# Optimization experiments

Measured on AMD Instinct MI355X. Metric: run time of the kernel, lower is better.

## Reference

```python
import jax, jax.numpy as jnp
import numpy as np

D = 2048
H = 16
HD = D // H
FF = 4 * D
B, L = 2, 2048
EPS = 1e-6
NEG = -1e9


def setup_inputs() -> dict:
    key = jax.random.key(0)
    ks = jax.random.split(key, 8)
    x = jax.random.normal(ks[0], (B, L, D), dtype=jnp.float32)
    # causal additive mask [1,1,L,L]
    causal = jnp.triu(jnp.full((L, L), NEG, dtype=jnp.float32), k=1)
    mask = causal[None, None, :, :]
    s = 0.02
    params = {
        'norm1_w': jnp.ones((D,), jnp.float32),
        'qkv_w': jax.random.normal(ks[1], (3 * D, D), jnp.float32) * s,
        'out_w': jax.random.normal(ks[2], (D, D), jnp.float32) * s,
        'norm2_w': jnp.ones((D,), jnp.float32),
        'gate_w': jax.random.normal(ks[3], (FF, D), jnp.float32) * s,
        'up_w': jax.random.normal(ks[4], (FF, D), jnp.float32) * s,
        'down_w': jax.random.normal(ks[5], (D, FF), jnp.float32) * s,
    }
    return {'x': x, 'mask': mask, **params}


def _rmsnorm(x, w):
    return x * jax.lax.rsqrt(jnp.mean(x * x, axis=-1, keepdims=True) + EPS) * w


def reference(x, mask, norm1_w, qkv_w, out_w, norm2_w, gate_w, up_w, down_w):
    b, l, d = x.shape
    # --- attention ---
    h = _rmsnorm(x, norm1_w)
    qkv = h @ qkv_w.T                          # [B,L,3D]
    qkv = qkv.reshape(b, l, 3, H, HD)
    q, k, v = (jnp.moveaxis(qkv, 2, 0)[i].transpose(0, 2, 1, 3) for i in range(3))  # each [B,H,L,HD]
    scores = jnp.einsum('bhqd,bhkd->bhqk', q, k) / jnp.sqrt(jnp.float32(HD))
    scores = scores + mask
    attn = jax.nn.softmax(scores, axis=-1)
    o = jnp.einsum('bhqk,bhkd->bhqd', attn, v)  # [B,H,L,HD]
    o = o.transpose(0, 2, 1, 3).reshape(b, l, d)
    x = x + o @ out_w.T
    # --- SwiGLU FFN ---
    h2 = _rmsnorm(x, norm2_w)
    ff = (jax.nn.silu(h2 @ gate_w.T) * (h2 @ up_w.T)) @ down_w.T
    return x + ff
```

## Files before the change

### kernel.cpp

```cpp
#include <hip/hip_runtime.h>


typedef __attribute__((ext_vector_type(8))) short bf16x8;
typedef __attribute__((ext_vector_type(4))) float f32x4;

__device__ __forceinline__ float b2f(unsigned short u) {
    return __uint_as_float(((unsigned int)u) << 16);
}
__device__ __forceinline__ unsigned short f2b(float f) {
    unsigned int i = __float_as_uint(f);
    i += 0x7fffu + ((i >> 16) & 1u);
    return (unsigned short)(i >> 16);
}
__device__ __forceinline__ unsigned int cvt_pk_bf16(float lo, float hi) {
    unsigned int r;
    asm("v_cvt_pk_bf16_f32 %0, %1, %2" : "=v"(r) : "v"(lo), "v"(hi));
    return r;
}

__device__ __forceinline__ void gload_lds16(const unsigned short* g, unsigned short* l) {
    __builtin_amdgcn_global_load_lds(
        (const __attribute__((address_space(1))) unsigned int*)g,
        (__attribute__((address_space(3))) unsigned int*)l,
        16, 0, 0);
}

template<int DT> struct IO;
template<> struct IO<1> {
    static __device__ __forceinline__ void load8(const void* p, size_t i, float* o) {
        uint4 v = *(const uint4*)((const unsigned short*)p + i);
        const unsigned short* u = (const unsigned short*)&v;
#pragma unroll
        for (int e = 0; e < 8; e++) o[e] = b2f(u[e]);
    }
    static __device__ __forceinline__ float load1(const void* p, size_t i) {
        return b2f(((const unsigned short*)p)[i]);
    }
    static __device__ __forceinline__ void store1(void* p, size_t i, float v) {
        ((unsigned short*)p)[i] = f2b(v);
    }
};
template<> struct IO<0> {
    static __device__ __forceinline__ void load8(const void* p, size_t i, float* o) {
        float4 a = *(const float4*)((const float*)p + i);
        float4 b = *(const float4*)((const float*)p + i + 4);
        o[0]=a.x; o[1]=a.y; o[2]=a.z; o[3]=a.w;
        o[4]=b.x; o[5]=b.y; o[6]=b.z; o[7]=b.w;
    }
    static __device__ __forceinline__ float load1(const void* p, size_t i) {
        return ((const float*)p)[i];
    }
    static __device__ __forceinline__ void store1(void* p, size_t i, float v) {
        ((float*)p)[i] = v;
    }
};

__global__ __launch_bounds__(256) void detect_kernel(
    const unsigned int* __restrict__ x, int* __restrict__ flag)
{
    const int t = threadIdx.x;
    int cnt = 0;
    for (int i = t; i < 2048; i += 256) {
        unsigned int e = (x[i] >> 7) & 0xFFu;
        cnt += (e >= 100u && e <= 140u) ? 1 : 0;
    }
#pragma unroll
    for (int off = 32; off; off >>= 1) cnt += __shfl_xor(cnt, off);
    __shared__ int red[4];
    if ((t & 63) == 0) red[t >> 6] = cnt;
    __syncthreads();
    if (t == 0) {
        int tot = red[0] + red[1] + red[2] + red[3];
        flag[0] = (2 * tot > 2048) ? 1 : 0;
    }
}

template<int PID, int DTX, int DTW>
__global__ __launch_bounds__(256) void rmsnorm_kernel(
    const int* __restrict__ flag,
    const void* __restrict__ X,
    const void* __restrict__ Wn,
    unsigned short* __restrict__ Out)
{
    if (flag[0] != PID) return;
    const int row = blockIdx.x, t = threadIdx.x;
    float xf[8];
    IO<DTX>::load8(X, (size_t)row * 2048 + t * 8, xf);
    float ss = 0.f;
#pragma unroll
    for (int e = 0; e < 8; e++) ss += xf[e] * xf[e];
#pragma unroll
    for (int off = 32; off; off >>= 1) ss += __shfl_xor(ss, off);
    __shared__ float red[4];
    if ((t & 63) == 0) red[t >> 6] = ss;
    __syncthreads();
    float rr = rsqrtf((red[0] + red[1] + red[2] + red[3]) * (1.0f / 2048.0f) + 1e-6f);
    float wf[8];
    IO<DTW>::load8(Wn, (size_t)t * 8, wf);
    float y[8];
#pragma unroll
    for (int e = 0; e < 8; e++) y[e] = xf[e] * rr * wf[e];
    uint4 ov;
    ov.x = cvt_pk_bf16(y[0], y[1]);
    ov.y = cvt_pk_bf16(y[2], y[3]);
    ov.z = cvt_pk_bf16(y[4], y[5]);
    ov.w = cvt_pk_bf16(y[6], y[7]);
    *(uint4*)(Out + (size_t)row * 2048 + t * 8) = ov;
}

#define BM 128
#define BN 128
#define BKK 64

template<int PID, int DTW, int DTR, int DTC, int EPI>
__global__ __launch_bounds__(256) void gemm_bt(
    const int* __restrict__ flag,
    const unsigned short* __restrict__ A,
    const void* __restrict__ W, size_t woff, int ldw,
    const void* __restrict__ Res,
    void* __restrict__ C,
    int N, int K)
{
    if (flag[0] != PID) return;
    __shared__ unsigned short sA[BM * BKK];
    __shared__ unsigned short sB[BN * BKK];
    const int t = threadIdx.x;
    const int bm = blockIdx.x * BM, bn = blockIdx.y * BN;
    const int w = t >> 6, lane = t & 63, quad = lane >> 4, l16 = lane & 15;
    const int wm = (w & 1) * 64, wn = (w >> 1) * 64;

    const int srow = lane >> 3;
    const int sg   = (lane & 7) ^ srow;

    f32x4 acc[4][4];
#pragma unroll
    for (int mi = 0; mi < 4; mi++)
#pragma unroll
        for (int ni = 0; ni < 4; ni++) {
            f32x4 z = {0.f, 0.f, 0.f, 0.f};
            acc[mi][ni] = z;
        }

    for (int k0 = 0; k0 < K; k0 += BKK) {
#pragma unroll
        for (int i = 0; i < 4; i++) {
            const int r0 = w * 32 + i * 8;
            gload_lds16(A + (size_t)(bm + r0 + srow) * K + k0 + sg * 8,
                        &sA[r0 * BKK]);
        }
        if constexpr (DTW == 1) {
#pragma unroll
            for (int i = 0; i < 4; i++) {
                const int r0 = w * 32 + i * 8;
                gload_lds16((const unsigned short*)W + woff +
                                (size_t)(bn + r0 + srow) * ldw + k0 + sg * 8,
                            &sB[r0 * BKK]);
            }
        } else {
#pragma unroll
            for (int i = 0; i < 4; i++) {
                const int r0 = w * 32 + i * 8;
                const int r = r0 + srow;
                const float* gp = (const float*)W + woff +
                                  (size_t)(bn + r) * ldw + k0 + (lane & 7) * 8;
                float4 f0 = *(const float4*)gp;
                float4 f1 = *(const float4*)(gp + 4);
                uint4 wb;
                wb.x = cvt_pk_bf16(f0.x, f0.y);
                wb.y = cvt_pk_bf16(f0.z, f0.w);
                wb.z = cvt_pk_bf16(f1.x, f1.y);
                wb.w = cvt_pk_bf16(f1.z, f1.w);
                *(uint4*)&sB[r * BKK + (((lane & 7) ^ (r & 7)) * 8)] = wb;
            }
        }
        __syncthreads();

#pragma unroll
        for (int ks = 0; ks < 2; ks++) {
            bf16x8 af[4], bfr[4];
#pragma unroll
            for (int mi = 0; mi < 4; mi++) {
                const int r = wm + mi * 16 + l16;
                af[mi] = *(const bf16x8*)
                    &sA[r * BKK + (((ks * 4 + quad) ^ (r & 7)) * 8)];
            }
#pragma unroll
            for (int ni = 0; ni < 4; ni++) {
                const int r = wn + ni * 16 + l16;
                bfr[ni] = *(const bf16x8*)
                    &sB[r * BKK + (((ks * 4 + quad) ^ (r & 7)) * 8)];
            }
#pragma unroll
            for (int mi = 0; mi < 4; mi++)
#pragma unroll
                for (int ni = 0; ni < 4; ni++)
                    acc[mi][ni] = __builtin_amdgcn_mfma_f32_16x16x32_bf16(
                        af[mi], bfr[ni], acc[mi][ni], 0, 0, 0);
        }
        __syncthreads();
    }

#pragma unroll
    for (int mi = 0; mi < 4; mi++)
#pragma unroll
        for (int ni = 0; ni < 4; ni++)
#pragma unroll
            for (int r = 0; r < 4; r++) {
                const int row = bm + wm + mi * 16 + quad * 4 + r;
                const int col = bn + wn + ni * 16 + l16;
                const size_t idx = (size_t)row * N + col;
                float v = acc[mi][ni][r];
                if constexpr (EPI == 1) v += IO<DTR>::load1(Res, idx);
                if constexpr (EPI == 2) v = v / (1.f + __expf(-v));
                if constexpr (EPI == 3) v *= IO<DTR>::load1(Res, idx);
                IO<DTC>::store1(C, idx, v);
            }
}

__device__ __forceinline__ int vt_idx(int d, int kv) {
    return d * 72 + (kv ^ (d & 56));
}

template<int PID>
__global__ __launch_bounds__(256) void attn_kernel(
    const int* __restrict__ flag,
    const unsigned short* __restrict__ QKV,
    unsigned short* __restrict__ O)
{
    if (flag[0] != PID) return;
    __shared__ unsigned short sK[64 * 128];
    __shared__ unsigned short sVt[9280];
    __shared__ unsigned short sP[4][16 * 72];

    const int t = threadIdx.x;
    const int bh = blockIdx.x >> 4;
    const int jj = blockIdx.x & 15;
    const int b = bh >> 4, hh = bh & 15;
    const int w = t >> 6, lane = t & 63, quad = lane >> 4, l16 = lane & 15;

    const unsigned short* Qb = QKV + (size_t)(b * 2048) * 6144 + hh * 128;
    const unsigned short* Kb = Qb + 2048;
    const unsigned short* Vb = Qb + 4096;

    const int str = t >> 4;
    const int stc = (t & 15) * 8;

#pragma unroll
    for (int half = 0; half < 2; half++) {
        const int qt = half ? (31 - jj) : jj;
        const int qbase = qt * 64;

        bf16x8 qf[4];
        {
            const unsigned short* qp = Qb + (size_t)(qbase + w * 16 + l16) * 6144;
#pragma unroll
            for (int ks = 0; ks < 4; ks++)
                qf[ks] = *(const bf16x8*)(qp + ks * 32 + quad * 8);
        }

        float m[4], l[4];
#pragma unroll
        for (int r = 0; r < 4; r++) { m[r] = -1e30f; l[r] = 0.f; }
        f32x4 accO[8];
#pragma unroll
        for (int d0 = 0; d0 < 8; d0++) {
            f32x4 z = {0.f, 0.f, 0.f, 0.f};
            accO[d0] = z;
        }

        for (int tk = 0; tk <= qt; tk++) {
            const int kv0 = tk * 64;
            __syncthreads();
#pragma unroll
            for (int pass = 0; pass < 4; pass++) {
                const int rr = str + pass * 16;
                uint4 kv4 = *(const uint4*)(Kb + (size_t)(kv0 + rr) * 6144 + stc);
                *(uint4*)&sK[(rr * 128 + stc) ^ ((rr & 7) << 3)] = kv4;
                uint4 vv4 = *(const uint4*)(Vb + (size_t)(kv0 + rr) * 6144 + stc);
                const unsigned short* vu = (const unsigned short*)&vv4;
#pragma unroll
                for (int e = 0; e < 8; e++)
                    sVt[vt_idx(stc + e, rr)] = vu[e];
            }
            __syncthreads();

            const bool diag = (tk == qt);
            f32x4 s[4];
#pragma unroll
            for (int nf = 0; nf < 4; nf++) {
                f32x4 z = {0.f, 0.f, 0.f, 0.f};
                s[nf] = z;
                if (!(diag && nf > w)) {
#pragma unroll
                    for (int ks = 0; ks < 4; ks++) {
                        const int row = nf * 16 + l16;
                        bf16x8 kf = *(const bf16x8*)
                            &sK[(row * 128 + ks * 32 + quad * 8) ^ ((row & 7) << 3)];
                        s[nf] = __builtin_amdgcn_mfma_f32_16x16x32_bf16(qf[ks], kf, s[nf], 0, 0, 0);
                    }
                }
#pragma unroll
                for (int r = 0; r < 4; r++) s[nf][r] *= 0.08838834764831845f;
            }
            if (diag) {
#pragma unroll
                for (int nf = 0; nf < 4; nf++)
#pragma unroll
                    for (int r = 0; r < 4; r++)
                        if (nf * 16 + l16 > w * 16 + quad * 4 + r) s[nf][r] = -1e30f;
            }

            float alpha[4], rs[4];
#pragma unroll
            for (int r = 0; r < 4; r++) {
                float v = fmaxf(fmaxf(s[0][r], s[1][r]), fmaxf(s[2][r], s[3][r]));
                v = fmaxf(v, __shfl_xor(v, 1));
                v = fmaxf(v, __shfl_xor(v, 2));
                v = fmaxf(v, __shfl_xor(v, 4));
                v = fmaxf(v, __shfl_xor(v, 8));
                float mn = fmaxf(m[r], v);
                alpha[r] = __expf(m[r] - mn);
                m[r] = mn;
                rs[r] = 0.f;
            }
#pragma unroll
            for (int nf = 0; nf < 4; nf++)
#pragma unroll
                for (int r = 0; r < 4; r++) {
                    float p = __expf(s[nf][r] - m[r]);
                    rs[r] += p;
                    sP[w][(quad * 4 + r) * 72 + nf * 16 + l16] = f2b(p);
                }
#pragma unroll
            for (int r = 0; r < 4; r++) {
                float sum = rs[r];
                sum += __shfl_xor(sum, 1);
                sum += __shfl_xor(sum, 2);
                sum += __shfl_xor(sum, 4);
                sum += __shfl_xor(sum, 8);
                l[r] = l[r] * alpha[r] + sum;
            }
#pragma unroll
            for (int d0 = 0; d0 < 8; d0++)
#pragma unroll
                for (int r = 0; r < 4; r++) accO[d0][r] *= alpha[r];

#pragma unroll
            for (int ks = 0; ks < 2; ks++) {
                bf16x8 pa = *(const bf16x8*)&sP[w][l16 * 72 + ks * 32 + quad * 8];
#pragma unroll
                for (int d0 = 0; d0 < 8; d0++) {
                    bf16x8 vb = *(const bf16x8*)
                        &sVt[vt_idx(d0 * 16 + l16, ks * 32 + quad * 8)];
                    accO[d0] = __builtin_amdgcn_mfma_f32_16x16x32_bf16(pa, vb, accO[d0], 0, 0, 0);
                }
            }
        }

        float linv[4];
#pragma unroll
        for (int r = 0; r < 4; r++) linv[r] = 1.0f / l[r];
        unsigned short* Op = O + (size_t)(b * 2048 + qbase + w * 16) * 2048 + hh * 128;
#pragma unroll
        for (int d0 = 0; d0 < 8; d0++)
#pragma unroll
            for (int r = 0; r < 4; r++)
                Op[(size_t)(quad * 4 + r) * 2048 + d0 * 16 + l16] =
                    f2b(accO[d0][r] * linv[r]);
    }
}

template<int DT>
static void run_pipeline(const void* x, const void* n1w, const void* qkvw,
                         const void* outw, const void* n2w, const void* gatew,
                         const void* upw, const void* downw,
                         void* outp, char* ws, const int* flag, hipStream_t stream)
{
    const size_t MB = 1024 * 1024;
    unsigned short* qkv = (unsigned short*)(ws);
    unsigned short* x2  = (unsigned short*)(ws);
    unsigned short* h2  = (unsigned short*)(ws + 16 * MB);
    unsigned short* a   = (unsigned short*)(ws + 32 * MB);
    unsigned short* h   = (unsigned short*)(ws + 48 * MB);
    unsigned short* o   = (unsigned short*)(ws + 48 * MB);

    rmsnorm_kernel<DT, DT, DT><<<4096, 256, 0, stream>>>(flag, x, n1w, h);
    gemm_bt<DT, DT, 1, 1, 0><<<dim3(32, 48), 256, 0, stream>>>(
        flag, h, qkvw, 0, 2048, nullptr, qkv, 6144, 2048);
    attn_kernel<DT><<<512, 256, 0, stream>>>(flag, qkv, o);
    gemm_bt<DT, DT, DT, 1, 1><<<dim3(32, 16), 256, 0, stream>>>(
        flag, o, outw, 0, 2048, x, x2, 2048, 2048);
    rmsnorm_kernel<DT, 1, DT><<<4096, 256, 0, stream>>>(flag, x2, n2w, h2);
    gemm_bt<DT, DT, 1, 1, 2><<<dim3(32, 32), 256, 0, stream>>>(
        flag, h2, gatew, 0, 2048, nullptr, a, 4096, 2048);
    gemm_bt<DT, DT, 1, 1, 3><<<dim3(32, 32), 256, 0, stream>>>(
        flag, h2, upw, 0, 2048, a, a, 4096, 2048);
    gemm_bt<DT, DT, 1, 1, 1><<<dim3(32, 16), 256, 0, stream>>>(
        flag, a, downw, 0, 8192, x2, x2, 2048, 4096);
    gemm_bt<DT, DT, 1, 1, 2><<<dim3(32, 32), 256, 0, stream>>>(
        flag, h2, gatew, (size_t)4096 * 2048, 2048, nullptr, a, 4096, 2048);
    gemm_bt<DT, DT, 1, 1, 3><<<dim3(32, 32), 256, 0, stream>>>(
        flag, h2, upw, (size_t)4096 * 2048, 2048, a, a, 4096, 2048);
    gemm_bt<DT, DT, 1, DT, 1><<<dim3(32, 16), 256, 0, stream>>>(
        flag, a, downw, 4096, 8192, x2, outp, 2048, 4096);
}

extern "C" void kernel_launch(void* const* d_in, const int* in_sizes, int n_in,
                              void* d_out, int out_size, void* d_ws, size_t ws_size,
                              hipStream_t stream)
{
    const void* x      = d_in[0];
    const void* n1w    = d_in[2];
    const void* qkv_w  = d_in[3];
    const void* out_w  = d_in[4];
    const void* n2w    = d_in[5];
    const void* gate_w = d_in[6];
    const void* up_w   = d_in[7];
    const void* down_w = d_in[8];

    char* ws = (char*)d_ws;
    const size_t MB = 1024 * 1024;
    size_t flag_off = 64 * MB;
    if (ws_size < flag_off + 4) flag_off = (ws_size - 4) & ~(size_t)3;
    int* flag = (int*)(ws + flag_off);

    detect_kernel<<<1, 256, 0, stream>>>((const unsigned int*)x, flag);
    run_pipeline<0>(x, n1w, qkv_w, out_w, n2w, gate_w, up_w, down_w,
                    d_out, ws, flag, stream);
    run_pipeline<1>(x, n1w, qkv_w, out_w, n2w, gate_w, up_w, down_w,
                    d_out, ws, flag, stream);
}
```

Before: 1.290 ms.

## Add 256x256 double-buffered GEMM with XCD swizzle for bf16 path

Adds a new GEMM kernel for the bf16-input path. It uses 256x256 tiles over 512 threads, double-buffers LDS and interleaves the next tile's global->LDS loads with MFMA phases. Block indices are remapped so that consecutive tiles land on the same XCD. All bf16 GEMMs in the pipeline now use it, while the fp32 path keeps the old kernel. The larger tile raises reuse per byte loaded, but launches fewer workgroups (128–384) on the many CUs and adds barrier and register pressure.

```diff
diff --git a/kernel.cpp b/kernel.cpp
--- a/kernel.cpp
+++ b/kernel.cpp
@@ -106,6 +106,199 @@
     ov.z = cvt_pk_bf16(y[4], y[5]);
     ov.w = cvt_pk_bf16(y[6], y[7]);
     *(uint4*)(Out + (size_t)row * 2048 + t * 8) = ov;
+}
+
+#define TBM 256
+#define TBN 256
+#define TBK 64
+
+template<int PID, int EPI>
+__global__ __launch_bounds__(512, 2) void gemm8(
+    const int* __restrict__ flag,
+    const unsigned short* __restrict__ A,
+    const unsigned short* __restrict__ W, size_t woff, int ldw,
+    const unsigned short* __restrict__ Res,
+    unsigned short* __restrict__ C,
+    int N, int K, int gx)
+{
+    if (flag[0] != PID) return;
+    __shared__ unsigned short sA[2][TBM * TBK];
+    __shared__ unsigned short sB[2][TBN * TBK];
+
+    const int t = threadIdx.x;
+    const int nwg = gridDim.x;
+    const int q8 = nwg >> 3, r8 = nwg & 7;
+    const int xcd = blockIdx.x & 7, o = blockIdx.x >> 3;
+    const int swz = (xcd < r8 ? xcd * (q8 + 1) : r8 * (q8 + 1) + (xcd - r8) * q8) + o;
+    const int bm = (swz % gx) * TBM;
+    const int bn = (swz / gx) * TBN;
+
+    const int w = t >> 6, lane = t & 63, quad = lane >> 4, l16 = lane & 15;
+    const int wr = w >> 2, wc = w & 3;
+    const int sg = (lane & 7) ^ (lane >> 3);
+
+    const unsigned short* Ab = A + (size_t)(bm + w * 8 + (lane >> 3)) * K + sg * 8;
+    const unsigned short* Wb = W + woff + (size_t)(bn + w * 8 + (lane >> 3)) * ldw + sg * 8;
+    const int dstb = (w * 8) * TBK;
+
+    f32x4 acc[8][4];
+#pragma unroll
+    for (int mi = 0; mi < 8; mi++)
+#pragma unroll
+        for (int ni = 0; ni < 4; ni++) {
+            f32x4 z = {0.f, 0.f, 0.f, 0.f};
+            acc[mi][ni] = z;
+        }
+
+#define STAGE_A8(b, k0)                                                        \
+    {                                                                          \
+        _Pragma("unroll")                                                      \
+        for (int i = 0; i < 4; i++)                                            \
+            gload_lds16(Ab + (size_t)(i * 64) * K + (k0),                      \
+                        &sA[b][i * 64 * TBK + dstb]);                          \
+    }
+#define STAGE_B8(b, k0)                                                        \
+    {                                                                          \
+        _Pragma("unroll")                                                      \
+        for (int i = 0; i < 4; i++)                                            \
+            gload_lds16(Wb + (size_t)(i * 64) * ldw + (k0),                    \
+                        &sB[b][i * 64 * TBK + dstb]);                          \
+    }
+
+    STAGE_A8(0, 0)
+    STAGE_B8(0, 0)
+    asm volatile("s_waitcnt vmcnt(0)" ::: "memory");
+    asm volatile("s_barrier" ::: "memory");
+
+    const int NT = K / TBK;
+    bf16x8 bfr[4][2];
+
+    for (int T = 0; T < NT; T++) {
+        const int buf = T & 1;
+        const int k0n = (T + 1) * TBK;
+        const bool more = (T + 1 < NT);
+
+        if (more) STAGE_A8(buf ^ 1, k0n)
+#pragma unroll
+        for (int ni = 0; ni < 4; ni++) {
+            const int row = wc * 64 + ni * 16 + l16;
+#pragma unroll
+            for (int ks = 0; ks < 2; ks++)
+                bfr[ni][ks] = *(const bf16x8*)
+                    &sB[buf][row * TBK + (((ks * 4 + quad) ^ (row & 7)) * 8)];
+        }
+        {
+            bf16x8 af[2][2];
+#pragma unroll
+            for (int m2 = 0; m2 < 2; m2++) {
+                const int row = wr * 128 + (0 + m2) * 16 + l16;
+#pragma unroll
+                for (int ks = 0; ks < 2; ks++)
+                    af[m2][ks] = *(const bf16x8*)
+                        &sA[buf][row * TBK + (((ks * 4 + quad) ^ (row & 7)) * 8)];
+            }
+            __builtin_amdgcn_s_setprio(1);
+#pragma unroll
+            for (int m2 = 0; m2 < 2; m2++)
+#pragma unroll
+                for (int ks = 0; ks < 2; ks++)
+#pragma unroll
+                    for (int ni = 0; ni < 4; ni++)
+                        acc[0 + m2][ni] = __builtin_amdgcn_mfma_f32_16x16x32_bf16(
+                            af[m2][ks], bfr[ni][ks], acc[0 + m2][ni], 0, 0, 0);
+            __builtin_amdgcn_s_setprio(0);
+        }
+        asm volatile("s_barrier" ::: "memory");
+
+        if (more) STAGE_B8(buf ^ 1, k0n)
+        {
+            bf16x8 af[2][2];
+#pragma unroll
+            for (int m2 = 0; m2 < 2; m2++) {
+                const int row = wr * 128 + (2 + m2) * 16 + l16;
+#pragma unroll
+                for (int ks = 0; ks < 2; ks++)
+                    af[m2][ks] = *(const bf16x8*)
+                        &sA[buf][row * TBK + (((ks * 4 + quad) ^ (row & 7)) * 8)];
+            }
+            __builtin_amdgcn_s_setprio(1);
+#pragma unroll
+            for (int m2 = 0; m2 < 2; m2++)
+#pragma unroll
+                for (int ks = 0; ks < 2; ks++)
+#pragma unroll
+                    for (int ni = 0; ni < 4; ni++)
+                        acc[2 + m2][ni] = __builtin_amdgcn_mfma_f32_16x16x32_bf16(
+                            af[m2][ks], bfr[ni][ks], acc[2 + m2][ni], 0, 0, 0);
+            __builtin_amdgcn_s_setprio(0);
+        }
+        asm volatile("s_barrier" ::: "memory");
+
+        {
+            bf16x8 af[2][2];
+#pragma unroll
+            for (int m2 = 0; m2 < 2; m2++) {
+                const int row = wr * 128 + (4 + m2) * 16 + l16;
+#pragma unroll
+                for (int ks = 0; ks < 2; ks++)
+                    af[m2][ks] = *(const bf16x8*)
+                        &sA[buf][row * TBK + (((ks * 4 + quad) ^ (row & 7)) * 8)];
+            }
+            __builtin_amdgcn_s_setprio(1);
+#pragma unroll
+            for (int m2 = 0; m2 < 2; m2++)
+#pragma unroll
+                for (int ks = 0; ks < 2; ks++)
+#pragma unroll
+                    for (int ni = 0; ni < 4; ni++)
+                        acc[4 + m2][ni] = __builtin_amdgcn_mfma_f32_16x16x32_bf16(
+                            af[m2][ks], bfr[ni][ks], acc[4 + m2][ni], 0, 0, 0);
+            __builtin_amdgcn_s_setprio(0);
+        }
+        asm volatile("s_barrier" ::: "memory");
+
+        {
+            bf16x8 af[2][2];
+#pragma unroll
+            for (int m2 = 0; m2 < 2; m2++) {
+                const int row = wr * 128 + (6 + m2) * 16 + l16;
+#pragma unroll
+                for (int ks = 0; ks < 2; ks++)
+                    af[m2][ks] = *(const bf16x8*)
+                        &sA[buf][row * TBK + (((ks * 4 + quad) ^ (row & 7)) * 8)];
+            }
+            __builtin_amdgcn_s_setprio(1);
+#pragma unroll
+            for (int m2 = 0; m2 < 2; m2++)
+#pragma unroll
+                for (int ks = 0; ks < 2; ks++)
+#pragma unroll
+                    for (int ni = 0; ni < 4; ni++)
+                        acc[6 + m2][ni] = __builtin_amdgcn_mfma_f32_16x16x32_bf16(
+                            af[m2][ks], bfr[ni][ks], acc[6 + m2][ni], 0, 0, 0);
+            __builtin_amdgcn_s_setprio(0);
+        }
+        asm volatile("s_waitcnt vmcnt(0)" ::: "memory");
+        asm volatile("s_barrier" ::: "memory");
+    }
+#undef STAGE_A8
+#undef STAGE_B8
+
+#pragma unroll
+    for (int mi = 0; mi < 8; mi++)
+#pragma unroll
+        for (int ni = 0; ni < 4; ni++)
+#pragma unroll
+            for (int r = 0; r < 4; r++) {
+                const int row = bm + wr * 128 + mi * 16 + quad * 4 + r;
+                const int col = bn + wc * 64 + ni * 16 + l16;
+                const size_t idx = (size_t)row * N + col;
+                float v = acc[mi][ni][r];
+                if constexpr (EPI == 1) v += b2f(Res[idx]);
+                if constexpr (EPI == 2) v = v / (1.f + __expf(-v));
+                if constexpr (EPI == 3) v *= b2f(Res[idx]);
+                C[idx] = f2b(v);
+            }
 }
 
 #define BM 128
@@ -141,11 +334,12 @@
             acc[mi][ni] = z;
         }
 
+    const unsigned short* Ap = A;
     for (int k0 = 0; k0 < K; k0 += BKK) {
 #pragma unroll
         for (int i = 0; i < 4; i++) {
             const int r0 = w * 32 + i * 8;
-            gload_lds16(A + (size_t)(bm + r0 + srow) * K + k0 + sg * 8,
+            gload_lds16(Ap + (size_t)(bm + r0 + srow) * K + k0 + sg * 8,
                         &sA[r0 * BKK]);
         }
         if constexpr (DTW == 1) {
@@ -385,24 +579,51 @@
     unsigned short* o   = (unsigned short*)(ws + 48 * MB);
 
     rmsnorm_kernel<DT, DT, DT><<<4096, 256, 0, stream>>>(flag, x, n1w, h);
-    gemm_bt<DT, DT, 1, 1, 0><<<dim3(32, 48), 256, 0, stream>>>(
-        flag, h, qkvw, 0, 2048, nullptr, qkv, 6144, 2048);
-    attn_kernel<DT><<<512, 256, 0, stream>>>(flag, qkv, o);
-    gemm_bt<DT, DT, DT, 1, 1><<<dim3(32, 16), 256, 0, stream>>>(
-        flag, o, outw, 0, 2048, x, x2, 2048, 2048);
-    rmsnorm_kernel<DT, 1, DT><<<4096, 256, 0, stream>>>(flag, x2, n2w, h2);
-    gemm_bt<DT, DT, 1, 1, 2><<<dim3(32, 32), 256, 0, stream>>>(
-        flag, h2, gatew, 0, 2048, nullptr, a, 4096, 2048);
-    gemm_bt<DT, DT, 1, 1, 3><<<dim3(32, 32), 256, 0, stream>>>(
-        flag, h2, upw, 0, 2048, a, a, 4096, 2048);
-    gemm_bt<DT, DT, 1, 1, 1><<<dim3(32, 16), 256, 0, stream>>>(
-        flag, a, downw, 0, 8192, x2, x2, 2048, 4096);
-    gemm_bt<DT, DT, 1, 1, 2><<<dim3(32, 32), 256, 0, stream>>>(
-        flag, h2, gatew, (size_t)4096 * 2048, 2048, nullptr, a, 4096, 2048);
-    gemm_bt<DT, DT, 1, 1, 3><<<dim3(32, 32), 256, 0, stream>>>(
-        flag, h2, upw, (size_t)4096 * 2048, 2048, a, a, 4096, 2048);
-    gemm_bt<DT, DT, 1, DT, 1><<<dim3(32, 16), 256, 0, stream>>>(
-        flag, a, downw, 4096, 8192, x2, outp, 2048, 4096);
+
+    if constexpr (DT == 1) {
+        const unsigned short* Wq = (const unsigned short*)qkvw;
+        const unsigned short* Wo = (const unsigned short*)outw;
+        const unsigned short* Wg = (const unsigned short*)gatew;
+        const unsigned short* Wu = (const unsigned short*)upw;
+        const unsigned short* Wd = (const unsigned short*)downw;
+        gemm8<1, 0><<<384, 512, 0, stream>>>(
+            flag, h, Wq, 0, 2048, nullptr, qkv, 6144, 2048, 16);
+        attn_kernel<1><<<512, 256, 0, stream>>>(flag, qkv, o);
+        gemm8<1, 1><<<128, 512, 0, stream>>>(
+            flag, o, Wo, 0, 2048, (const unsigned short*)x, x2, 2048, 2048, 16);
+        rmsnorm_kernel<1, 1, 1><<<4096, 256, 0, stream>>>(flag, x2, n2w, h2);
+        gemm8<1, 2><<<256, 512, 0, stream>>>(
+            flag, h2, Wg, 0, 2048, nullptr, a, 4096, 2048, 16);
+        gemm8<1, 3><<<256, 512, 0, stream>>>(
+            flag, h2, Wu, 0, 2048, a, a, 4096, 2048, 16);
+        gemm8<1, 1><<<128, 512, 0, stream>>>(
+            flag, a, Wd, 0, 8192, x2, x2, 2048, 4096, 16);
+        gemm8<1, 2><<<256, 512, 0, stream>>>(
+            flag, h2, Wg, (size_t)4096 * 2048, 2048, nullptr, a, 4096, 2048, 16);
+        gemm8<1, 3><<<256, 512, 0, stream>>>(
+            flag, h2, Wu, (size_t)4096 * 2048, 2048, a, a, 4096, 2048, 16);
+        gemm8<1, 1><<<128, 512, 0, stream>>>(
+            flag, a, Wd, 4096, 8192, x2, (unsigned short*)outp, 2048, 4096, 16);
+    } else {
+        gemm_bt<0, 0, 1, 1, 0><<<dim3(32, 48), 256, 0, stream>>>(
+            flag, h, qkvw, 0, 2048, nullptr, qkv, 6144, 2048);
+        attn_kernel<0><<<512, 256, 0, stream>>>(flag, qkv, o);
+        gemm_bt<0, 0, 0, 1, 1><<<dim3(32, 16), 256, 0, stream>>>(
+            flag, o, outw, 0, 2048, x, x2, 2048, 2048);
+        rmsnorm_kernel<0, 1, 0><<<4096, 256, 0, stream>>>(flag, x2, n2w, h2);
+        gemm_bt<0, 0, 1, 1, 2><<<dim3(32, 32), 256, 0, stream>>>(
+            flag, h2, gatew, 0, 2048, nullptr, a, 4096, 2048);
+        gemm_bt<0, 0, 1, 1, 3><<<dim3(32, 32), 256, 0, stream>>>(
+            flag, h2, upw, 0, 2048, a, a, 4096, 2048);
+        gemm_bt<0, 0, 1, 1, 1><<<dim3(32, 16), 256, 0, stream>>>(
+            flag, a, downw, 0, 8192, x2, x2, 2048, 4096);
+        gemm_bt<0, 0, 1, 1, 2><<<dim3(32, 32), 256, 0, stream>>>(
+            flag, h2, gatew, (size_t)4096 * 2048, 2048, nullptr, a, 4096, 2048);
+        gemm_bt<0, 0, 1, 1, 3><<<dim3(32, 32), 256, 0, stream>>>(
+            flag, h2, upw, (size_t)4096 * 2048, 2048, a, a, 4096, 2048);
+        gemm_bt<0, 0, 1, 0, 1><<<dim3(32, 16), 256, 0, stream>>>(
+            flag, a, downw, 4096, 8192, x2, outp, 2048, 4096);
+    }
 }
 
 extern "C" void kernel_launch(void* const* d_in, const int* in_sizes, int n_in,
```

New measurement: 1.287 ms. No clear change (-0.2%).

## Replace GEMM with triple-buffered 512-thread kernel and pre-convert fp32 weights

Applied to the files above, without the earlier changes.

Replaces the single-buffered 128x128 GEMM with a 512-thread kernel using 256-wide N tiles, BK=32 and a three-stage global-to-LDS pipeline with explicit vmcnt waits. It also adds an XCD-aware block swizzle and raises MFMA priority around the math. For fp32 weights, a separate conversion kernel writes bf16 copies into scratch (reusing the output and h2 buffers) before each GEMM, instead of converting inside the tile loop. This adds extra weight read and write traffic, and reusing those buffers depends on the kernels running in order.

```diff
diff --git a/kernel.cpp b/kernel.cpp
--- a/kernel.cpp
+++ b/kernel.cpp
@@ -73,6 +73,28 @@
         int tot = red[0] + red[1] + red[2] + red[3];
         flag[0] = (2 * tot > 2048) ? 1 : 0;
     }
+}
+
+template<int PID>
+__global__ __launch_bounds__(256) void convw_kernel(
+    const int* __restrict__ flag,
+    const float* __restrict__ S, int lds_,
+    unsigned short* __restrict__ D, int ldd,
+    int total)
+{
+    if (flag[0] != PID) return;
+    const int i = (blockIdx.x * 256 + threadIdx.x) * 8;
+    if (i >= total) return;
+    const int row = i / ldd, col = i - row * ldd;
+    const float* sp = S + (size_t)row * lds_ + col;
+    float4 f0 = *(const float4*)sp;
+    float4 f1 = *(const float4*)(sp + 4);
+    uint4 ov;
+    ov.x = cvt_pk_bf16(f0.x, f0.y);
+    ov.y = cvt_pk_bf16(f0.z, f0.w);
+    ov.z = cvt_pk_bf16(f1.x, f1.y);
+    ov.w = cvt_pk_bf16(f1.z, f1.w);
+    *(uint4*)(D + i) = ov;
 }
 
 template<int PID, int DTX, int DTW>
@@ -108,106 +130,110 @@
     *(uint4*)(Out + (size_t)row * 2048 + t * 8) = ov;
 }
 
-#define BM 128
-#define BN 128
-#define BKK 64
-
-template<int PID, int DTW, int DTR, int DTC, int EPI>
-__global__ __launch_bounds__(256) void gemm_bt(
+template<int PID, int TBMX, int DTR, int DTC, int EPI>
+__global__ __launch_bounds__(512, 2) void gemm3(
     const int* __restrict__ flag,
     const unsigned short* __restrict__ A,
-    const void* __restrict__ W, size_t woff, int ldw,
+    const unsigned short* __restrict__ W, size_t woff, int ldw,
     const void* __restrict__ Res,
     void* __restrict__ C,
-    int N, int K)
+    int N, int K, int gx)
 {
     if (flag[0] != PID) return;
-    __shared__ unsigned short sA[BM * BKK];
-    __shared__ unsigned short sB[BN * BKK];
+    constexpr int MF  = TBMX / 32;
+    constexpr int ACH = TBMX / 128;
+    constexpr int LPT = ACH + 2;
+    __shared__ unsigned short sA[3][TBMX * 32];
+    __shared__ unsigned short sB[3][256 * 32];
+
     const int t = threadIdx.x;
-    const int bm = blockIdx.x * BM, bn = blockIdx.y * BN;
+    const int nwg = gridDim.x;
+    const int q8 = nwg >> 3, r8 = nwg & 7;
+    const int xcd = blockIdx.x & 7, oo = blockIdx.x >> 3;
+    const int swz = (xcd < r8 ? xcd * (q8 + 1) : r8 * (q8 + 1) + (xcd - r8) * q8) + oo;
+    const int bm = (swz % gx) * TBMX;
+    const int bn = (swz / gx) * 256;
+
     const int w = t >> 6, lane = t & 63, quad = lane >> 4, l16 = lane & 15;
-    const int wm = (w & 1) * 64, wn = (w >> 1) * 64;
-
-    const int srow = lane >> 3;
-    const int sg   = (lane & 7) ^ srow;
-
-    f32x4 acc[4][4];
-#pragma unroll
-    for (int mi = 0; mi < 4; mi++)
+    const int wr = w >> 2, wc = w & 3;
+    const int swr = (l16 ^ (l16 >> 2)) & 3;
+
+    const int srow = w * 16 + (lane >> 2);
+    const int sgr  = (((t & 3) ^ ((lane >> 2) & 3) ^ quad) << 3);
+    const unsigned short* Abase = A + (size_t)(bm + srow) * K + sgr;
+    const unsigned short* Wbase = W + woff + (size_t)(bn + srow) * ldw + sgr;
+    const int ldst = w * 512;
+
+    f32x4 acc[MF][4];
+#pragma unroll
+    for (int mi = 0; mi < MF; mi++)
 #pragma unroll
         for (int ni = 0; ni < 4; ni++) {
             f32x4 z = {0.f, 0.f, 0.f, 0.f};
             acc[mi][ni] = z;
         }
 
-    for (int k0 = 0; k0 < K; k0 += BKK) {
-#pragma unroll
-        for (int i = 0; i < 4; i++) {
-            const int r0 = w * 32 + i * 8;
-            gload_lds16(A + (size_t)(bm + r0 + srow) * K + k0 + sg * 8,
-                        &sA[r0 * BKK]);
-        }
-        if constexpr (DTW == 1) {
-#pragma unroll
-            for (int i = 0; i < 4; i++) {
-                const int r0 = w * 32 + i * 8;
-                gload_lds16((const unsigned short*)W + woff +
-                                (size_t)(bn + r0 + srow) * ldw + k0 + sg * 8,
-                            &sB[r0 * BKK]);
-            }
+#define STG(bb, T)                                                             \
+    do {                                                                       \
+        const size_t ko = (size_t)(T) * 32;                                    \
+        _Pragma("unroll")                                                      \
+        for (int c = 0; c < ACH; c++)                                          \
+            gload_lds16(Abase + (size_t)(c * 128) * K + ko,                    \
+                        &sA[bb][c * 4096 + ldst]);                             \
+        _Pragma("unroll")                                                      \
+        for (int c = 0; c < 2; c++)                                            \
+            gload_lds16(Wbase + (size_t)(c * 128) * ldw + ko,                  \
+                        &sB[bb][c * 4096 + ldst]);                             \
+    } while (0)
+
+    STG(0, 0);
+    STG(1, 1);
+
+    const int NT = K / 32;
+    for (int T = 0; T < NT; T++) {
+        if (T + 1 < NT) {
+            if constexpr (LPT == 4)
+                asm volatile("s_waitcnt vmcnt(4)" ::: "memory");
+            else
+                asm volatile("s_waitcnt vmcnt(3)" ::: "memory");
         } else {
-#pragma unroll
-            for (int i = 0; i < 4; i++) {
-                const int r0 = w * 32 + i * 8;
-                const int r = r0 + srow;
-                const float* gp = (const float*)W + woff +
-                                  (size_t)(bn + r) * ldw + k0 + (lane & 7) * 8;
-                float4 f0 = *(const float4*)gp;
-                float4 f1 = *(const float4*)(gp + 4);
-                uint4 wb;
-                wb.x = cvt_pk_bf16(f0.x, f0.y);
-                wb.y = cvt_pk_bf16(f0.z, f0.w);
-                wb.z = cvt_pk_bf16(f1.x, f1.y);
-                wb.w = cvt_pk_bf16(f1.z, f1.w);
-                *(uint4*)&sB[r * BKK + (((lane & 7) ^ (r & 7)) * 8)] = wb;
-            }
-        }
-        __syncthreads();
-
-#pragma unroll
-        for (int ks = 0; ks < 2; ks++) {
-            bf16x8 af[4], bfr[4];
-#pragma unroll
-            for (int mi = 0; mi < 4; mi++) {
-                const int r = wm + mi * 16 + l16;
-                af[mi] = *(const bf16x8*)
-                    &sA[r * BKK + (((ks * 4 + quad) ^ (r & 7)) * 8)];
-            }
-#pragma unroll
-            for (int ni = 0; ni < 4; ni++) {
-                const int r = wn + ni * 16 + l16;
-                bfr[ni] = *(const bf16x8*)
-                    &sB[r * BKK + (((ks * 4 + quad) ^ (r & 7)) * 8)];
-            }
-#pragma unroll
-            for (int mi = 0; mi < 4; mi++)
-#pragma unroll
-                for (int ni = 0; ni < 4; ni++)
-                    acc[mi][ni] = __builtin_amdgcn_mfma_f32_16x16x32_bf16(
-                        af[mi], bfr[ni], acc[mi][ni], 0, 0, 0);
-        }
-        __syncthreads();
-    }
-
-#pragma unroll
-    for (int mi = 0; mi < 4; mi++)
+            asm volatile("s_waitcnt vmcnt(0)" ::: "memory");
+        }
+        asm volatile("s_barrier" ::: "memory");
+        if (T + 2 < NT) STG((T + 2) % 3, T + 2);
+
+        const unsigned short* a_ = sA[T % 3];
+        const unsigned short* b_ = sB[T % 3];
+        bf16x8 af[MF], bfr[4];
+#pragma unroll
+        for (int ni = 0; ni < 4; ni++) {
+            const int row = wc * 64 + ni * 16 + l16;
+            bfr[ni] = *(const bf16x8*)&b_[row * 32 + ((quad ^ swr) << 3)];
+        }
+#pragma unroll
+        for (int mi = 0; mi < MF; mi++) {
+            const int row = wr * (TBMX / 2) + mi * 16 + l16;
+            af[mi] = *(const bf16x8*)&a_[row * 32 + ((quad ^ swr) << 3)];
+        }
+        __builtin_amdgcn_s_setprio(1);
+#pragma unroll
+        for (int mi = 0; mi < MF; mi++)
+#pragma unroll
+            for (int ni = 0; ni < 4; ni++)
+                acc[mi][ni] = __builtin_amdgcn_mfma_f32_16x16x32_bf16(
+                    af[mi], bfr[ni], acc[mi][ni], 0, 0, 0);
+        __builtin_amdgcn_s_setprio(0);
+    }
+#undef STG
+
+#pragma unroll
+    for (int mi = 0; mi < MF; mi++)
 #pragma unroll
         for (int ni = 0; ni < 4; ni++)
 #pragma unroll
             for (int r = 0; r < 4; r++) {
-                const int row = bm + wm + mi * 16 + quad * 4 + r;
-                const int col = bn + wn + ni * 16 + l16;
+                const int row = bm + wr * (TBMX / 2) + mi * 16 + quad * 4 + r;
+                const int col = bn + wc * 64 + ni * 16 + l16;
                 const size_t idx = (size_t)row * N + col;
                 float v = acc[mi][ni][r];
                 if constexpr (EPI == 1) v += IO<DTR>::load1(Res, idx);
@@ -385,24 +411,70 @@
     unsigned short* o   = (unsigned short*)(ws + 48 * MB);
 
     rmsnorm_kernel<DT, DT, DT><<<4096, 256, 0, stream>>>(flag, x, n1w, h);
-    gemm_bt<DT, DT, 1, 1, 0><<<dim3(32, 48), 256, 0, stream>>>(
-        flag, h, qkvw, 0, 2048, nullptr, qkv, 6144, 2048);
-    attn_kernel<DT><<<512, 256, 0, stream>>>(flag, qkv, o);
-    gemm_bt<DT, DT, DT, 1, 1><<<dim3(32, 16), 256, 0, stream>>>(
-        flag, o, outw, 0, 2048, x, x2, 2048, 2048);
-    rmsnorm_kernel<DT, 1, DT><<<4096, 256, 0, stream>>>(flag, x2, n2w, h2);
-    gemm_bt<DT, DT, 1, 1, 2><<<dim3(32, 32), 256, 0, stream>>>(
-        flag, h2, gatew, 0, 2048, nullptr, a, 4096, 2048);
-    gemm_bt<DT, DT, 1, 1, 3><<<dim3(32, 32), 256, 0, stream>>>(
-        flag, h2, upw, 0, 2048, a, a, 4096, 2048);
-    gemm_bt<DT, DT, 1, 1, 1><<<dim3(32, 16), 256, 0, stream>>>(
-        flag, a, downw, 0, 8192, x2, x2, 2048, 4096);
-    gemm_bt<DT, DT, 1, 1, 2><<<dim3(32, 32), 256, 0, stream>>>(
-        flag, h2, gatew, (size_t)4096 * 2048, 2048, nullptr, a, 4096, 2048);
-    gemm_bt<DT, DT, 1, 1, 3><<<dim3(32, 32), 256, 0, stream>>>(
-        flag, h2, upw, (size_t)4096 * 2048, 2048, a, a, 4096, 2048);
-    gemm_bt<DT, DT, 1, DT, 1><<<dim3(32, 16), 256, 0, stream>>>(
-        flag, a, downw, 4096, 8192, x2, outp, 2048, 4096);
+
+    if constexpr (DT == 1) {
+        const unsigned short* Wq = (const unsigned short*)qkvw;
+        const unsigned short* Wo = (const unsigned short*)outw;
+        const unsigned short* Wg = (const unsigned short*)gatew;
+        const unsigned short* Wu = (const unsigned short*)upw;
+        const unsigned short* Wd = (const unsigned short*)downw;
+        gemm3<1, 256, 1, 1, 0><<<384, 512, 0, stream>>>(
+            flag, h, Wq, 0, 2048, nullptr, qkv, 6144, 2048, 16);
+        attn_kernel<1><<<512, 256, 0, stream>>>(flag, qkv, o);
+        gemm3<1, 128, 1, 1, 1><<<256, 512, 0, stream>>>(
+            flag, o, Wo, 0, 2048, x, x2, 2048, 2048, 32);
+        rmsnorm_kernel<1, 1, 1><<<4096, 256, 0, stream>>>(flag, x2, n2w, h2);
+        gemm3<1, 256, 1, 1, 2><<<256, 512, 0, stream>>>(
+            flag, h2, Wg, 0, 2048, nullptr, a, 4096, 2048, 16);
+        gemm3<1, 256, 1, 1, 3><<<256, 512, 0, stream>>>(
+            flag, h2, Wu, 0, 2048, a, a, 4096, 2048, 16);
+        gemm3<1, 128, 1, 1, 1><<<256, 512, 0, stream>>>(
+            flag, a, Wd, 0, 8192, x2, x2, 2048, 4096, 32);
+        gemm3<1, 256, 1, 1, 2><<<256, 512, 0, stream>>>(
+            flag, h2, Wg, (size_t)4096 * 2048, 2048, nullptr, a, 4096, 2048, 16);
+        gemm3<1, 256, 1, 1, 3><<<256, 512, 0, stream>>>(
+            flag, h2, Wu, (size_t)4096 * 2048, 2048, a, a, 4096, 2048, 16);
+        gemm3<1, 128, 1, 1, 1><<<256, 512, 0, stream>>>(
+            flag, a, Wd, 4096, 8192, x2, outp, 2048, 4096, 32);
+    } else {
+        unsigned short* WC  = (unsigned short*)outp;
+        unsigned short* WC2 = h2;
+
+        convw_kernel<0><<<6144, 256, 0, stream>>>(
+            flag, (const float*)qkvw, 2048, WC, 2048, 6144 * 2048);
+        gemm3<0, 256, 1, 1, 0><<<384, 512, 0, stream>>>(
+            flag, h, WC, 0, 2048, nullptr, qkv, 6144, 2048, 16);
+        attn_kernel<0><<<512, 256, 0, stream>>>(flag, qkv, o);
+        convw_kernel<0><<<2048, 256, 0, stream>>>(
+            flag, (const float*)outw, 2048, WC, 2048, 2048 * 2048);
+        gemm3<0, 128, 0, 1, 1><<<256, 512, 0, stream>>>(
+            flag, o, WC, 0, 2048, x, x2, 2048, 2048, 32);
+        rmsnorm_kernel<0, 1, 0><<<4096, 256, 0, stream>>>(flag, x2, n2w, h2);
+        convw_kernel<0><<<4096, 256, 0, stream>>>(
+            flag, (const float*)gatew, 2048, WC, 2048, 4096 * 2048);
+        gemm3<0, 256, 1, 1, 2><<<256, 512, 0, stream>>>(
+            flag, h2, WC, 0, 2048, nullptr, a, 4096, 2048, 16);
+        convw_kernel<0><<<4096, 256, 0, stream>>>(
+            flag, (const float*)upw, 2048, WC, 2048, 4096 * 2048);
+        gemm3<0, 256, 1, 1, 3><<<256, 512, 0, stream>>>(
+            flag, h2, WC, 0, 2048, a, a, 4096, 2048, 16);
+        convw_kernel<0><<<4096, 256, 0, stream>>>(
+            flag, (const float*)downw, 8192, WC, 4096, 2048 * 4096);
+        gemm3<0, 128, 1, 1, 1><<<256, 512, 0, stream>>>(
+            flag, a, WC, 0, 4096, x2, x2, 2048, 4096, 32);
+        convw_kernel<0><<<4096, 256, 0, stream>>>(
+            flag, (const float*)gatew + (size_t)4096 * 2048, 2048, WC, 2048, 4096 * 2048);
+        gemm3<0, 256, 1, 1, 2><<<256, 512, 0, stream>>>(
+            flag, h2, WC, 0, 2048, nullptr, a, 4096, 2048, 16);
+        convw_kernel<0><<<4096, 256, 0, stream>>>(
+            flag, (const float*)upw + (size_t)4096 * 2048, 2048, WC, 2048, 4096 * 2048);
+        gemm3<0, 256, 1, 1, 3><<<256, 512, 0, stream>>>(
+            flag, h2, WC, 0, 2048, a, a, 4096, 2048, 16);
+        convw_kernel<0><<<4096, 256, 0, stream>>>(
+            flag, (const float*)downw + 4096, 8192, WC2, 4096, 2048 * 4096);
+        gemm3<0, 128, 1, 0, 1><<<256, 512, 0, stream>>>(
+            flag, a, WC2, 0, 4096, x2, outp, 2048, 4096, 32);
+    }
 }
 
 extern "C" void kernel_launch(void* const* d_in, const int* in_sizes, int n_in,
```

After: 1.294 ms. Within noise of the previous version (+0.3%).
